# Performance work log

Measured on AMD Instinct MI355X. Metric: run time of the kernel, lower is better.

Reference implementation:

```python
import jax, jax.numpy as jnp
import numpy as np

B, N_H, N_W, DIM, HEADS = 2, 64, 64, 768, 12
HINT = 1024
HIDDEN = DIM * 2       # LTRM expand_ratio = 2
K_ECA = 5              # ECA kernel for C=768: int(|log2(768)/2 + 0.5|)=5 (odd)
TH_LO, TH_HI, MIN_EDGE = 0.02, 0.98, 64


def setup_inputs() -> dict:
    key = jax.random.key(0)
    ks = jax.random.split(key, 12)
    N = N_H * N_W
    x = jax.random.normal(ks[0], (B, N, DIM), jnp.float32)
    # alpha hint: left half = uniform noise (uncertain -> edge tokens),
    # right half = binary blocks aligned to the 16px token cells (easy tokens)
    blocks = (jax.random.uniform(ks[1], (B, 1, N_H, N_W)) > 0.5).astype(jnp.float32)
    blocks_up = jnp.repeat(jnp.repeat(blocks, HINT // N_H, axis=2), HINT // N_W, axis=3)
    noise = jax.random.uniform(ks[2], (B, 1, HINT, HINT))
    col = jnp.arange(HINT)[None, None, None, :]
    alpha_hint = jnp.where(col < HINT // 2, noise, blocks_up)
    s = 0.02
    return {
        "x": x,
        "alpha_hint": alpha_hint,
        # global attention (Hiera-style patched MaskUnitAttention, q_stride=1)
        "qkv_w": jax.random.normal(ks[3], (DIM, 3 * DIM), jnp.float32) * s,
        "qkv_b": jnp.zeros((3 * DIM,), jnp.float32),
        "proj_w": jax.random.normal(ks[4], (DIM, DIM), jnp.float32) * s,
        "proj_b": jnp.zeros((DIM,), jnp.float32),
        # LTRM
        "ln_g": jnp.ones((DIM,), jnp.float32),
        "ln_b": jnp.zeros((DIM,), jnp.float32),
        "fc1_w": jax.random.normal(ks[5], (DIM, HIDDEN), jnp.float32) * s,
        "fc1_b": jnp.zeros((HIDDEN,), jnp.float32),
        "fc2_w": jax.random.normal(ks[6], (HIDDEN, DIM), jnp.float32) * s,  # zeros in ckpt; random for non-trivial math
        "fc2_b": jnp.zeros((DIM,), jnp.float32),
        "eca_w": jax.random.normal(ks[7], (K_ECA,), jnp.float32) * 0.2,
    }


def _edge_mask(alpha_hint):
    # F.interpolate(mode='area') with exact integer factor == block mean
    Bn = alpha_hint.shape[0]
    f_h, f_w = HINT // N_H, HINT // N_W
    hint = alpha_hint.reshape(Bn, N_H, f_h, N_W, f_w).mean(axis=(2, 4)).reshape(Bn, N_H * N_W)
    edge = (hint > TH_LO) & (hint < TH_HI)
    # per-batch fallback: too few edge tokens -> route everything to attention
    edge = jnp.where(edge.sum(axis=1, keepdims=True) < MIN_EDGE, True, edge)
    return edge  # [B, N] bool


def _layernorm(h, g, b, eps=1e-5):
    mu = h.mean(-1, keepdims=True)
    var = ((h - mu) ** 2).mean(-1, keepdims=True)
    return (h - mu) * jax.lax.rsqrt(var + eps) * g + b


def reference(x, alpha_hint, qkv_w, qkv_b, proj_w, proj_b,
              ln_g, ln_b, fc1_w, fc1_b, fc2_w, fc2_b, eca_w):
    Bn, N, C = x.shape
    hd = C // HEADS
    edge = _edge_mask(alpha_hint)                      # [B, N] bool

    # ---- edge path: global SDPA restricted to edge tokens (masked form of
    # the gather->attend->scatter routing: same math, edge keys only) ----
    qkv = (x @ qkv_w + qkv_b).reshape(Bn, N, 3, HEADS, hd)
    q = qkv[:, :, 0].transpose(0, 2, 1, 3)             # [B,H,N,hd]
    k = qkv[:, :, 1].transpose(0, 2, 1, 3)
    v = qkv[:, :, 2].transpose(0, 2, 1, 3)
    scores = jnp.einsum('bhqd,bhkd->bhqk', q, k) / jnp.sqrt(jnp.asarray(hd, x.dtype))
    scores = scores + jnp.where(edge[:, None, None, :], 0.0, -1e9).astype(x.dtype)
    attn = jax.nn.softmax(scores, axis=-1)
    o = jnp.einsum('bhqk,bhkd->bhqd', attn, v)
    o = o.transpose(0, 2, 1, 3).reshape(Bn, N, C)
    attn_out = x + (o @ proj_w + proj_b)               # residual around attention

    # ---- easy path: LTRM (subset of tokens -> DWConv branch skipped,
    # exactly as in LTRM.forward when N != H*W) ----
    h = _layernorm(x, ln_g, ln_b)
    h = jax.nn.gelu(h @ fc1_w + fc1_b, approximate=False)
    h = jax.nn.gelu(h, approximate=False)
    h = h @ fc2_w + fc2_b                              # [B,N,C]
    # ECA: avg-pool over the routed (easy) token set -> masked mean
    easy = ~edge
    cnt = jnp.maximum(easy.sum(axis=1).astype(x.dtype), 1.0)      # [B]
    pooled = (h * easy[..., None]).sum(axis=1) / cnt[:, None]     # [B,C]
    g = jax.lax.conv_general_dilated(
        pooled[:, None, :], eca_w.reshape(1, 1, K_ECA), (1,), 'SAME',
        dimension_numbers=('NCH', 'OIH', 'NCH'))[:, 0, :]          # [B,C]
    h = h * jax.nn.sigmoid(g)[:, None, :]
    ltrm_out = x + h

    # ---- scatter-combine ----
    return jnp.where(edge[..., None], attn_out, ltrm_out)
```

## Files before the change

kernel.cpp:

```cpp
#include <hip/hip_runtime.h>

using u16 = unsigned short;
using short8 = __attribute__((ext_vector_type(8))) short;
using f32x4 = __attribute__((ext_vector_type(4))) float;

#define NTOK 4096
#define CDIM 768
#define QKVD 2304
#define NHEAD 12

__device__ __forceinline__ u16 f2bf(float f) {
  unsigned u = __float_as_uint(f);
  u += 0x7FFFu + ((u >> 16) & 1u);
  return (u16)(u >> 16);
}

__device__ __forceinline__ void gload_lds16(const void* g, void* l) {
  __builtin_amdgcn_global_load_lds(
      (__attribute__((address_space(1))) void*)g,
      (__attribute__((address_space(3))) void*)l, 16u, 0, 0u);
}

__device__ __forceinline__ float gelu_exact(float z) {
  return 0.5f * z * (1.0f + erff(z * 0.70710678118654752f));
}

__global__ __launch_bounds__(256) void pool_hint_kernel(
    const float* __restrict__ ah, float* __restrict__ hint)
{
  const int bid = blockIdx.x;
  const int b = bid >> 6, cr = bid & 63;
  const int t = threadIdx.x;
  const float* base = ah + ((size_t)b * 1024 + (size_t)cr * 16) * 1024;
  float s = 0.f;
#pragma unroll
  for (int pr = 0; pr < 16; ++pr) {
    float4 v = *(const float4*)(base + (size_t)pr * 1024 + t * 4);
    s += v.x + v.y + v.z + v.w;
  }
  s += __shfl_xor(s, 1);
  s += __shfl_xor(s, 2);
  if ((t & 3) == 0)
    hint[b * NTOK + cr * 64 + (t >> 2)] = s * (1.f / 256.f);
}

__global__ __launch_bounds__(1024) void finalize_edge_kernel(
    const float* __restrict__ hint, int* __restrict__ edge,
    int* __restrict__ qidx, int* __restrict__ ecnt)
{
  const int b = blockIdx.x, t = threadIdx.x;
  __shared__ int wsum[16];
  __shared__ int scnt;
  __shared__ int stot;
  int bits[4]; int s = 0;
#pragma unroll
  for (int j = 0; j < 4; ++j) {
    float h = hint[b * NTOK + t * 4 + j];
    bits[j] = (h > 0.02f && h < 0.98f) ? 1 : 0;
    s += bits[j];
    qidx[b * NTOK + t * 4 + j] = -1;
  }
  int sw = s;
#pragma unroll
  for (int d = 1; d < 64; d <<= 1) sw += __shfl_xor(sw, d);
  const int l = t & 63, w = t >> 6;
  if (l == 0) wsum[w] = sw;
  if (t == 0) scnt = 0;
  __syncthreads();
  if (t == 0) { int a = 0; for (int i = 0; i < 16; ++i) a += wsum[i]; stot = a; }
  __syncthreads();
  const int cnt = stot;
  const bool fb = cnt < 64;
#pragma unroll
  for (int j = 0; j < 4; ++j) {
    int e = fb ? 1 : bits[j];
    edge[b * NTOK + t * 4 + j] = e;
    if (e) {
      int p = atomicAdd(&scnt, 1);
      qidx[b * NTOK + p] = t * 4 + j;
    }
  }
  if (t == 0) ecnt[b] = fb ? 0 : (NTOK - cnt);
}

__global__ __launch_bounds__(256) void ln_kernel(
    const float* __restrict__ x, const float* __restrict__ gam,
    const float* __restrict__ bet, u16* __restrict__ lnb, u16* __restrict__ xb)
{
  const int row = blockIdx.x, t = threadIdx.x;
  const float* xr = x + (size_t)row * CDIM;
  float v[3];
#pragma unroll
  for (int j = 0; j < 3; ++j) v[j] = xr[t + j * 256];
  float s = v[0] + v[1] + v[2];
  float ss = v[0] * v[0] + v[1] * v[1] + v[2] * v[2];
#pragma unroll
  for (int d = 1; d < 64; d <<= 1) { s += __shfl_xor(s, d); ss += __shfl_xor(ss, d); }
  __shared__ float red[8];
  const int l = t & 63, w = t >> 6;
  if (l == 0) { red[w * 2] = s; red[w * 2 + 1] = ss; }
  __syncthreads();
  s = red[0] + red[2] + red[4] + red[6];
  ss = red[1] + red[3] + red[5] + red[7];
  const float mu = s * (1.f / 768.f);
  const float rstd = rsqrtf(ss * (1.f / 768.f) - mu * mu + 1e-5f);
#pragma unroll
  for (int j = 0; j < 3; ++j) {
    const int cc = t + j * 256;
    lnb[(size_t)row * CDIM + cc] = f2bf((v[j] - mu) * rstd * gam[cc] + bet[cc]);
    xb[(size_t)row * CDIM + cc] = f2bf(v[j]);
  }
}

__global__ __launch_bounds__(256) void transpose_kernel(
    const float* __restrict__ in, u16* __restrict__ outp, int K, int N)
{
  __shared__ float tile[32][33];
  const int bx = blockIdx.x, by = blockIdx.y;
  const int tx = threadIdx.x & 31, ty = threadIdx.x >> 5;
#pragma unroll
  for (int j = 0; j < 32; j += 8)
    tile[ty + j][tx] = in[(size_t)(by * 32 + ty + j) * N + bx * 32 + tx];
  __syncthreads();
#pragma unroll
  for (int j = 0; j < 32; j += 8)
    outp[(size_t)(bx * 32 + ty + j) * K + by * 32 + tx] = f2bf(tile[tx][ty + j]);
}

template <int EPI>
__global__ __launch_bounds__(256) void gemm_bt(
    const u16* __restrict__ A, const u16* __restrict__ Bt,
    const float* __restrict__ bias, const float* __restrict__ resid,
    void* __restrict__ outp, int M, int N, int K)
{
  __shared__ __align__(16) u16 lA[128 * 32];
  __shared__ __align__(16) u16 lB[128 * 32];
  const int t = threadIdx.x;
  const int l = t & 63, w = t >> 6;
  const int g = l >> 4, c = l & 15;
  const int wr = w >> 1, wc = w & 1;
  const int bm = blockIdx.x, bn = blockIdx.y;

  f32x4 acc[4][4];
#pragma unroll
  for (int i = 0; i < 4; ++i)
#pragma unroll
    for (int j = 0; j < 4; ++j) acc[i][j] = f32x4{0.f, 0.f, 0.f, 0.f};

  const int srow = t >> 2;
  const int sslot = (t & 3) ^ (srow & 3);
  const u16* gA0 = A + (size_t)(bm * 128 + srow) * K + sslot * 8;
  const u16* gA1 = A + (size_t)(bm * 128 + 64 + srow) * K + sslot * 8;
  const u16* gB0 = Bt + (size_t)(bn * 128 + srow) * K + sslot * 8;
  const u16* gB1 = Bt + (size_t)(bn * 128 + 64 + srow) * K + sslot * 8;
  char* ldA = (char*)lA + w * 1024;
  char* ldB = (char*)lB + w * 1024;

  for (int k0 = 0; k0 < K; k0 += 32) {
    __syncthreads();
    gload_lds16(gA0 + k0, ldA);
    gload_lds16(gA1 + k0, ldA + 4096);
    gload_lds16(gB0 + k0, ldB);
    gload_lds16(gB1 + k0, ldB + 4096);
    __syncthreads();
    short8 af[4], bfr[4];
#pragma unroll
    for (int mi = 0; mi < 4; ++mi) {
      int row = wr * 64 + mi * 16 + c;
      af[mi] = *(const short8*)((const char*)lA + row * 64 + ((g ^ (row & 3)) << 4));
    }
#pragma unroll
    for (int ni = 0; ni < 4; ++ni) {
      int row = wc * 64 + ni * 16 + c;
      bfr[ni] = *(const short8*)((const char*)lB + row * 64 + ((g ^ (row & 3)) << 4));
    }
#pragma unroll
    for (int mi = 0; mi < 4; ++mi)
#pragma unroll
      for (int ni = 0; ni < 4; ++ni)
        acc[mi][ni] = __builtin_amdgcn_mfma_f32_16x16x32_bf16(af[mi], bfr[ni], acc[mi][ni], 0, 0, 0);
  }

#pragma unroll
  for (int mi = 0; mi < 4; ++mi) {
#pragma unroll
    for (int ni = 0; ni < 4; ++ni) {
      const int col = bn * 128 + wc * 64 + ni * 16 + c;
      const float bv = bias[col];
      const int row0 = bm * 128 + wr * 64 + mi * 16 + g * 4;
#pragma unroll
      for (int r = 0; r < 4; ++r) {
        float v = acc[mi][ni][r] + bv;
        const size_t idx = (size_t)(row0 + r) * N + col;
        if constexpr (EPI == 0) {
          ((u16*)outp)[idx] = f2bf(v);
        } else if constexpr (EPI == 1) {
          ((float*)outp)[idx] = v + resid[idx];
        } else if constexpr (EPI == 2) {
          ((u16*)outp)[idx] = f2bf(gelu_exact(gelu_exact(v)));
        } else {
          ((float*)outp)[idx] = v;
        }
      }
    }
  }
}

__global__ __launch_bounds__(256) void flash_kernel(
    const u16* __restrict__ qkv, const int* __restrict__ qidx, u16* __restrict__ o)
{
  const int qt = blockIdx.x;
  const int bh = blockIdx.y;
  const int b = bh / NHEAD, h = bh % NHEAD;
  const int* qx = qidx + b * NTOK;
  if (qx[qt * 128] < 0) return;

  __shared__ __align__(16) u16 lK[64 * 64];
  __shared__ __align__(16) u16 lV[64 * 64];
  __shared__ __align__(16) u16 lP[4][32 * 64];

  const int t = threadIdx.x;
  const int l = t & 63, w = t >> 6;
  const int g = l >> 4, c = l & 15;
  const size_t tokbase = (size_t)b * NTOK;

  short8 qf[2][2];
#pragma unroll
  for (int mi = 0; mi < 2; ++mi) {
    int qi = qx[qt * 128 + w * 32 + mi * 16 + c];
    if (qi < 0) qi = 0;
    const u16* qp = qkv + (tokbase + qi) * QKVD + h * 64;
#pragma unroll
    for (int kb = 0; kb < 2; ++kb)
      qf[mi][kb] = *(const short8*)(qp + kb * 32 + g * 8);
  }

  f32x4 oacc[2][4];
  float mrun[2][4], lrun[2][4];
#pragma unroll
  for (int mi = 0; mi < 2; ++mi) {
#pragma unroll
    for (int nd = 0; nd < 4; ++nd) oacc[mi][nd] = f32x4{0.f, 0.f, 0.f, 0.f};
#pragma unroll
    for (int r = 0; r < 4; ++r) { mrun[mi][r] = -1e30f; lrun[mi][r] = 0.f; }
  }

  u16* lPw = lP[w];

  for (int kt = 0; kt < NTOK / 64; ++kt) {
    if (qx[kt * 64] < 0) break;
    __syncthreads();
#pragma unroll
    for (int j = 0; j < 2; ++j) {
      int seg = j * 256 + t;
      int row = seg >> 3;
      int sl = (seg & 7) ^ (row & 7);
      int ki = qx[kt * 64 + row]; if (ki < 0) ki = 0;
      gload_lds16(qkv + (tokbase + ki) * QKVD + CDIM + h * 64 + sl * 8,
                  (char*)lK + j * 4096 + w * 1024);
    }
    {
      int vi = qx[kt * 64 + l]; if (vi < 0) vi = 0;
      const u16* vg = qkv + (tokbase + vi) * QKVD + 2 * CDIM + h * 64 + w * 16;
      union { uint4 q[2]; u16 s[16]; } vv;
      vv.q[0] = *(const uint4*)(vg);
      vv.q[1] = *(const uint4*)(vg + 8);
#pragma unroll
      for (int jj = 0; jj < 16; ++jj) {
        int d = w * 16 + jj;
        *(u16*)((char*)lV + d * 128 + ((l * 2) ^ ((d & 7) << 4))) = vv.s[jj];
      }
    }
    __syncthreads();

    short8 kf[4][2];
#pragma unroll
    for (int ni = 0; ni < 4; ++ni) {
      int row = ni * 16 + c;
#pragma unroll
      for (int kb = 0; kb < 2; ++kb)
        kf[ni][kb] = *(const short8*)((const char*)lK + row * 128 + (((kb * 4 + g) ^ (row & 7)) << 4));
    }
    f32x4 s[2][4];
#pragma unroll
    for (int mi = 0; mi < 2; ++mi)
#pragma unroll
      for (int ni = 0; ni < 4; ++ni) {
        f32x4 sv = f32x4{0.f, 0.f, 0.f, 0.f};
        sv = __builtin_amdgcn_mfma_f32_16x16x32_bf16(qf[mi][0], kf[ni][0], sv, 0, 0, 0);
        sv = __builtin_amdgcn_mfma_f32_16x16x32_bf16(qf[mi][1], kf[ni][1], sv, 0, 0, 0);
        s[mi][ni] = sv;
      }

    float emask[4];
#pragma unroll
    for (int ni = 0; ni < 4; ++ni)
      emask[ni] = (qx[kt * 64 + ni * 16 + c] >= 0) ? 0.f : -1e9f;

#pragma unroll
    for (int mi = 0; mi < 2; ++mi) {
      float mx[4];
#pragma unroll
      for (int r = 0; r < 4; ++r) {
        float a0 = s[mi][0][r] * 0.125f + emask[0];
        float a1 = s[mi][1][r] * 0.125f + emask[1];
        float a2 = s[mi][2][r] * 0.125f + emask[2];
        float a3 = s[mi][3][r] * 0.125f + emask[3];
        s[mi][0][r] = a0; s[mi][1][r] = a1; s[mi][2][r] = a2; s[mi][3][r] = a3;
        mx[r] = fmaxf(fmaxf(a0, a1), fmaxf(a2, a3));
      }
#pragma unroll
      for (int r = 0; r < 4; ++r)
#pragma unroll
        for (int d = 1; d < 16; d <<= 1)
          mx[r] = fmaxf(mx[r], __shfl_xor(mx[r], d));

      float alpha[4], rs[4];
#pragma unroll
      for (int r = 0; r < 4; ++r) {
        float mnew = fmaxf(mrun[mi][r], mx[r]);
        alpha[r] = __expf(mrun[mi][r] - mnew);
        mrun[mi][r] = mnew;
        float accp = 0.f;
        const int prow = mi * 16 + g * 4 + r;
#pragma unroll
        for (int ni = 0; ni < 4; ++ni) {
          float p = __expf(s[mi][ni][r] - mnew);
          accp += p;
          *(u16*)((char*)lPw + prow * 128 + (((ni * 16 + c) * 2) ^ ((prow & 7) << 4))) = f2bf(p);
        }
        rs[r] = accp;
      }
#pragma unroll
      for (int r = 0; r < 4; ++r)
#pragma unroll
        for (int d = 1; d < 16; d <<= 1) rs[r] += __shfl_xor(rs[r], d);
#pragma unroll
      for (int r = 0; r < 4; ++r) {
        lrun[mi][r] = lrun[mi][r] * alpha[r] + rs[r];
#pragma unroll
        for (int nd = 0; nd < 4; ++nd) oacc[mi][nd][r] *= alpha[r];
      }
    }

#pragma unroll
    for (int kb = 0; kb < 2; ++kb) {
      short8 pa[2], vf[4];
#pragma unroll
      for (int mi = 0; mi < 2; ++mi) {
        int prow = mi * 16 + c;
        pa[mi] = *(const short8*)((const char*)lPw + prow * 128 + (((kb * 4 + g) ^ (prow & 7)) << 4));
      }
#pragma unroll
      for (int nd = 0; nd < 4; ++nd) {
        int vrow = nd * 16 + c;
        vf[nd] = *(const short8*)((const char*)lV + vrow * 128 + (((kb * 4 + g) ^ (vrow & 7)) << 4));
      }
#pragma unroll
      for (int mi = 0; mi < 2; ++mi)
#pragma unroll
        for (int nd = 0; nd < 4; ++nd)
          oacc[mi][nd] = __builtin_amdgcn_mfma_f32_16x16x32_bf16(pa[mi], vf[nd], oacc[mi][nd], 0, 0, 0);
    }
  }

#pragma unroll
  for (int mi = 0; mi < 2; ++mi) {
    float inv[4];
#pragma unroll
    for (int r = 0; r < 4; ++r) inv[r] = 1.f / lrun[mi][r];
#pragma unroll
    for (int r = 0; r < 4; ++r) {
      int oi = qx[qt * 128 + w * 32 + mi * 16 + g * 4 + r];
      if (oi >= 0) {
        u16* op = o + (tokbase + oi) * CDIM + h * 64;
#pragma unroll
        for (int nd = 0; nd < 4; ++nd)
          op[nd * 16 + c] = f2bf(oacc[mi][nd][r] * inv[r]);
      }
    }
  }
}

__global__ __launch_bounds__(256) void pool_partial_kernel(
    const float* __restrict__ h2, const int* __restrict__ edge, float* __restrict__ pooled)
{
  const int bid = blockIdx.x;
  const int b = bid / 48, rm = bid % 48;
  const int cg = rm / 16, ts = rm % 16;
  const int ch = cg * 256 + threadIdx.x;
  float s = 0.f;
  for (int tok = ts * 256; tok < ts * 256 + 256; ++tok) {
    if (!edge[b * NTOK + tok])
      s += h2[((size_t)b * NTOK + tok) * CDIM + ch];
  }
  atomicAdd(&pooled[b * CDIM + ch], s);
}

__global__ void eca_kernel(const float* __restrict__ pooled, const float* __restrict__ w5,
                           const int* __restrict__ ecnt, float* __restrict__ gate)
{
  const int b = blockIdx.x, c = threadIdx.x;
  const float inv = 1.f / fmaxf((float)ecnt[b], 1.f);
  float a = 0.f;
#pragma unroll
  for (int j = 0; j < 5; ++j) {
    int i = c - 2 + j;
    if (i >= 0 && i < CDIM) a += w5[j] * pooled[b * CDIM + i];
  }
  a *= inv;
  gate[b * CDIM + c] = 1.f / (1.f + __expf(-a));
}

__global__ __launch_bounds__(256) void combine_kernel(
    const float* __restrict__ x, const float* __restrict__ attn,
    const float* __restrict__ h2, const float* __restrict__ gate,
    const int* __restrict__ edge, float* __restrict__ out)
{
  const size_t i = ((size_t)blockIdx.x * 256 + threadIdx.x) * 4;
  const int b = (int)(i / ((size_t)NTOK * CDIM));
  const size_t r = i % ((size_t)NTOK * CDIM);
  const int tok = (int)(r / CDIM);
  const int cc = (int)(r % CDIM);
  float4 ov;
  if (edge[b * NTOK + tok]) {
    ov = *(const float4*)(attn + i);
  } else {
    float4 xv = *(const float4*)(x + i);
    float4 hv = *(const float4*)(h2 + i);
    float4 gv = *(const float4*)(gate + b * CDIM + cc);
    ov.x = xv.x + hv.x * gv.x;
    ov.y = xv.y + hv.y * gv.y;
    ov.z = xv.z + hv.z * gv.z;
    ov.w = xv.w + hv.w * gv.w;
  }
  *(float4*)(out + i) = ov;
}

extern "C" void kernel_launch(void* const* d_in, const int* in_sizes, int n_in,
                              void* d_out, int out_size, void* d_ws, size_t ws_size,
                              hipStream_t stream) {
  const float* x      = (const float*)d_in[0];
  const float* ah     = (const float*)d_in[1];
  const float* qkv_w  = (const float*)d_in[2];
  const float* qkv_b  = (const float*)d_in[3];
  const float* proj_w = (const float*)d_in[4];
  const float* proj_b = (const float*)d_in[5];
  const float* ln_g   = (const float*)d_in[6];
  const float* ln_b   = (const float*)d_in[7];
  const float* fc1_w  = (const float*)d_in[8];
  const float* fc1_b  = (const float*)d_in[9];
  const float* fc2_w  = (const float*)d_in[10];
  const float* fc2_b  = (const float*)d_in[11];
  const float* eca_w  = (const float*)d_in[12];
  float* out = (float*)d_out;

  char* ws = (char*)d_ws;
  size_t off = 0;
  auto alloc = [&](size_t bytes) {
    char* p = ws + off;
    off += (bytes + 255) & ~(size_t)255;
    return p;
  };
  float* hint   = (float*)alloc((size_t)2 * NTOK * 4);
  int*   edge   = (int*)alloc((size_t)2 * NTOK * 4);
  int*   qidx   = (int*)alloc((size_t)2 * NTOK * 4);
  int*   ecnt   = (int*)alloc(256);
  u16*   xbf    = (u16*)alloc((size_t)2 * NTOK * CDIM * 2);
  u16*   lnbf   = (u16*)alloc((size_t)2 * NTOK * CDIM * 2);
  u16*   qkvT   = (u16*)alloc((size_t)QKVD * CDIM * 2);
  u16*   projT  = (u16*)alloc((size_t)CDIM * CDIM * 2);
  u16*   fc1T   = (u16*)alloc((size_t)1536 * CDIM * 2);
  u16*   fc2T   = (u16*)alloc((size_t)CDIM * 1536 * 2);
  u16*   qkvb   = (u16*)alloc((size_t)2 * NTOK * QKVD * 2);
  u16*   obf    = (u16*)alloc((size_t)2 * NTOK * CDIM * 2);
  u16*   h1bf   = (u16*)alloc((size_t)2 * NTOK * 1536 * 2);
  float* h2     = (float*)alloc((size_t)2 * NTOK * CDIM * 4);
  float* attn   = (float*)alloc((size_t)2 * NTOK * CDIM * 4);
  float* pooled = (float*)alloc((size_t)2 * CDIM * 4);
  float* gate   = (float*)alloc((size_t)2 * CDIM * 4);

  pool_hint_kernel<<<dim3(128), 256, 0, stream>>>(ah, hint);
  finalize_edge_kernel<<<dim3(2), 1024, 0, stream>>>(hint, edge, qidx, ecnt);
  ln_kernel<<<dim3(8192), 256, 0, stream>>>(x, ln_g, ln_b, lnbf, xbf);
  transpose_kernel<<<dim3(72, 24), 256, 0, stream>>>(qkv_w, qkvT, 768, 2304);
  transpose_kernel<<<dim3(24, 24), 256, 0, stream>>>(proj_w, projT, 768, 768);
  transpose_kernel<<<dim3(48, 24), 256, 0, stream>>>(fc1_w, fc1T, 768, 1536);
  transpose_kernel<<<dim3(24, 48), 256, 0, stream>>>(fc2_w, fc2T, 1536, 768);

  gemm_bt<0><<<dim3(64, 18), 256, 0, stream>>>(xbf, qkvT, qkv_b, nullptr, qkvb, 8192, 2304, 768);
  flash_kernel<<<dim3(32, 24), 256, 0, stream>>>(qkvb, qidx, obf);
  gemm_bt<1><<<dim3(64, 6), 256, 0, stream>>>(obf, projT, proj_b, x, attn, 8192, 768, 768);
  gemm_bt<2><<<dim3(64, 12), 256, 0, stream>>>(lnbf, fc1T, fc1_b, nullptr, h1bf, 8192, 1536, 768);
  gemm_bt<3><<<dim3(64, 6), 256, 0, stream>>>(h1bf, fc2T, fc2_b, nullptr, h2, 8192, 768, 1536);

  hipMemsetAsync(pooled, 0, (size_t)2 * CDIM * 4, stream);
  pool_partial_kernel<<<dim3(96), 256, 0, stream>>>(h2, edge, pooled);
  eca_kernel<<<dim3(2), 768, 0, stream>>>(pooled, eca_w, ecnt, gate);
  combine_kernel<<<dim3(6144), 256, 0, stream>>>(x, attn, h2, gate, edge, out);
}
```

Baseline: 553.3 us.

## Compact edge/easy token lists so GEMMs skip unused rows; split-KV flash attention

Token routing now builds two compacted index lists, one for edge tokens and one for easy tokens. The QKV and fc1 GEMMs gather only the routed rows, and the proj and fc2 GEMMs scatter results back by token index. Tiles with no routed rows exit early, which roughly halves the matmul work. Flash attention now reads the compacted QKV contiguously and splits the key range into two partitions, adding a merge kernel that combines partial outputs with their max and sum statistics. The trade-off is extra partial-output buffers, an extra launch and list indirection inside the GEMM loads and epilogues.

```diff
diff --git a/kernel.cpp b/kernel.cpp
--- a/kernel.cpp
+++ b/kernel.cpp
@@ -13,6 +13,9 @@
   unsigned u = __float_as_uint(f);
   u += 0x7FFFu + ((u >> 16) & 1u);
   return (u16)(u >> 16);
+}
+__device__ __forceinline__ float bf2f(u16 v) {
+  return __uint_as_float(((unsigned)v) << 16);
 }
 
 __device__ __forceinline__ void gload_lds16(const void* g, void* l) {
@@ -46,12 +49,12 @@
 
 __global__ __launch_bounds__(1024) void finalize_edge_kernel(
     const float* __restrict__ hint, int* __restrict__ edge,
-    int* __restrict__ qidx, int* __restrict__ ecnt)
+    int* __restrict__ qidx, int* __restrict__ eidx,
+    int* __restrict__ cntE, int* __restrict__ cntZ)
 {
   const int b = blockIdx.x, t = threadIdx.x;
   __shared__ int wsum[16];
-  __shared__ int scnt;
-  __shared__ int stot;
+  __shared__ int scntE, scntZ, stot;
   int bits[4]; int s = 0;
 #pragma unroll
   for (int j = 0; j < 4; ++j) {
@@ -59,28 +62,32 @@
     bits[j] = (h > 0.02f && h < 0.98f) ? 1 : 0;
     s += bits[j];
     qidx[b * NTOK + t * 4 + j] = -1;
+    eidx[b * NTOK + t * 4 + j] = -1;
   }
   int sw = s;
 #pragma unroll
   for (int d = 1; d < 64; d <<= 1) sw += __shfl_xor(sw, d);
   const int l = t & 63, w = t >> 6;
   if (l == 0) wsum[w] = sw;
-  if (t == 0) scnt = 0;
+  if (t == 0) { scntE = 0; scntZ = 0; }
   __syncthreads();
   if (t == 0) { int a = 0; for (int i = 0; i < 16; ++i) a += wsum[i]; stot = a; }
   __syncthreads();
-  const int cnt = stot;
-  const bool fb = cnt < 64;
+  const bool fb = stot < 64;
 #pragma unroll
   for (int j = 0; j < 4; ++j) {
     int e = fb ? 1 : bits[j];
     edge[b * NTOK + t * 4 + j] = e;
     if (e) {
-      int p = atomicAdd(&scnt, 1);
+      int p = atomicAdd(&scntE, 1);
       qidx[b * NTOK + p] = t * 4 + j;
-    }
-  }
-  if (t == 0) ecnt[b] = fb ? 0 : (NTOK - cnt);
+    } else {
+      int p = atomicAdd(&scntZ, 1);
+      eidx[b * NTOK + p] = t * 4 + j;
+    }
+  }
+  __syncthreads();
+  if (t == 0) { cntE[b] = scntE; cntZ[b] = scntZ; }
 }
 
 __global__ __launch_bounds__(256) void ln_kernel(
@@ -127,19 +134,23 @@
     outp[(size_t)(bx * 32 + ty + j) * K + by * 32 + tx] = f2bf(tile[tx][ty + j]);
 }
 
-template <int EPI>
+template <int EPI, bool GATHER_A, bool SCATTER_OUT>
 __global__ __launch_bounds__(256) void gemm_bt(
     const u16* __restrict__ A, const u16* __restrict__ Bt,
     const float* __restrict__ bias, const float* __restrict__ resid,
-    void* __restrict__ outp, int M, int N, int K)
-{
+    const int* __restrict__ list, void* __restrict__ outp, int N, int K)
+{
+  const int bm = blockIdx.x, bn = blockIdx.y;
+  const int b = bm >> 5, bmi = bm & 31;
+  const int rb = bmi * 128;
+  if (list[b * NTOK + rb] < 0) return;
+
   __shared__ __align__(16) u16 lA[128 * 32];
   __shared__ __align__(16) u16 lB[128 * 32];
   const int t = threadIdx.x;
   const int l = t & 63, w = t >> 6;
   const int g = l >> 4, c = l & 15;
   const int wr = w >> 1, wc = w & 1;
-  const int bm = blockIdx.x, bn = blockIdx.y;
 
   f32x4 acc[4][4];
 #pragma unroll
@@ -149,8 +160,16 @@
 
   const int srow = t >> 2;
   const int sslot = (t & 3) ^ (srow & 3);
-  const u16* gA0 = A + (size_t)(bm * 128 + srow) * K + sslot * 8;
-  const u16* gA1 = A + (size_t)(bm * 128 + 64 + srow) * K + sslot * 8;
+  int ta0, ta1;
+  if constexpr (GATHER_A) {
+    ta0 = list[b * NTOK + rb + srow];       if (ta0 < 0) ta0 = 0;
+    ta1 = list[b * NTOK + rb + 64 + srow];  if (ta1 < 0) ta1 = 0;
+  } else {
+    ta0 = rb + srow;
+    ta1 = rb + 64 + srow;
+  }
+  const u16* gA0 = A + ((size_t)b * NTOK + ta0) * K + sslot * 8;
+  const u16* gA1 = A + ((size_t)b * NTOK + ta1) * K + sslot * 8;
   const u16* gB0 = Bt + (size_t)(bn * 128 + srow) * K + sslot * 8;
   const u16* gB1 = Bt + (size_t)(bn * 128 + 64 + srow) * K + sslot * 8;
   char* ldA = (char*)lA + w * 1024;
@@ -187,11 +206,19 @@
     for (int ni = 0; ni < 4; ++ni) {
       const int col = bn * 128 + wc * 64 + ni * 16 + c;
       const float bv = bias[col];
-      const int row0 = bm * 128 + wr * 64 + mi * 16 + g * 4;
+      const int prow0 = rb + wr * 64 + mi * 16 + g * 4;
 #pragma unroll
       for (int r = 0; r < 4; ++r) {
         float v = acc[mi][ni][r] + bv;
-        const size_t idx = (size_t)(row0 + r) * N + col;
+        int orow;
+        if constexpr (SCATTER_OUT) {
+          int tok = list[b * NTOK + prow0 + r];
+          if (tok < 0) continue;
+          orow = tok;
+        } else {
+          orow = prow0 + r;
+        }
+        const size_t idx = ((size_t)b * NTOK + orow) * N + col;
         if constexpr (EPI == 0) {
           ((u16*)outp)[idx] = f2bf(v);
         } else if constexpr (EPI == 1) {
@@ -206,14 +233,22 @@
   }
 }
 
-__global__ __launch_bounds__(256) void flash_kernel(
-    const u16* __restrict__ qkv, const int* __restrict__ qidx, u16* __restrict__ o)
+#define NSPLIT 2
+__global__ __launch_bounds__(256) void flash_part_kernel(
+    const u16* __restrict__ qkv, const int* __restrict__ cntE,
+    u16* __restrict__ partO, float2* __restrict__ partML)
 {
   const int qt = blockIdx.x;
   const int bh = blockIdx.y;
+  const int sp = blockIdx.z;
   const int b = bh / NHEAD, h = bh % NHEAD;
-  const int* qx = qidx + b * NTOK;
-  if (qx[qt * 128] < 0) return;
+  const int cnt = cntE[b];
+  if (qt * 128 >= cnt) return;
+
+  const int ntiles = (cnt + 63) >> 6;
+  const int half = (ntiles + NSPLIT - 1) / NSPLIT;
+  const int tA = sp * half;
+  const int tB = min(ntiles, tA + half);
 
   __shared__ __align__(16) u16 lK[64 * 64];
   __shared__ __align__(16) u16 lV[64 * 64];
@@ -227,9 +262,8 @@
   short8 qf[2][2];
 #pragma unroll
   for (int mi = 0; mi < 2; ++mi) {
-    int qi = qx[qt * 128 + w * 32 + mi * 16 + c];
-    if (qi < 0) qi = 0;
-    const u16* qp = qkv + (tokbase + qi) * QKVD + h * 64;
+    const int pos = qt * 128 + w * 32 + mi * 16 + c;
+    const u16* qp = qkv + (tokbase + pos) * QKVD + h * 64;
 #pragma unroll
     for (int kb = 0; kb < 2; ++kb)
       qf[mi][kb] = *(const short8*)(qp + kb * 32 + g * 8);
@@ -247,28 +281,27 @@
 
   u16* lPw = lP[w];
 
-  for (int kt = 0; kt < NTOK / 64; ++kt) {
-    if (qx[kt * 64] < 0) break;
+  for (int kt = tA; kt < tB; ++kt) {
     __syncthreads();
 #pragma unroll
     for (int j = 0; j < 2; ++j) {
       int seg = j * 256 + t;
       int row = seg >> 3;
       int sl = (seg & 7) ^ (row & 7);
-      int ki = qx[kt * 64 + row]; if (ki < 0) ki = 0;
-      gload_lds16(qkv + (tokbase + ki) * QKVD + CDIM + h * 64 + sl * 8,
+      gload_lds16(qkv + (tokbase + kt * 64 + row) * QKVD + CDIM + h * 64 + sl * 8,
                   (char*)lK + j * 4096 + w * 1024);
     }
     {
-      int vi = qx[kt * 64 + l]; if (vi < 0) vi = 0;
-      const u16* vg = qkv + (tokbase + vi) * QKVD + 2 * CDIM + h * 64 + w * 16;
-      union { uint4 q[2]; u16 s[16]; } vv;
-      vv.q[0] = *(const uint4*)(vg);
-      vv.q[1] = *(const uint4*)(vg + 8);
-#pragma unroll
-      for (int jj = 0; jj < 16; ++jj) {
-        int d = w * 16 + jj;
-        *(u16*)((char*)lV + d * 128 + ((l * 2) ^ ((d & 7) << 4))) = vv.s[jj];
+      const int kp = t & 31, db = t >> 5;
+      const u16* vg = qkv + (tokbase + kt * 64 + kp * 2) * QKVD + 2 * CDIM + h * 64 + db * 8;
+      union { uint4 q; u16 s[8]; } v0, v1;
+      v0.q = *(const uint4*)vg;
+      v1.q = *(const uint4*)(vg + QKVD);
+#pragma unroll
+      for (int j = 0; j < 8; ++j) {
+        int d = db * 8 + j;
+        unsigned pk = (unsigned)v0.s[j] | ((unsigned)v1.s[j] << 16);
+        *(unsigned*)((char*)lV + d * 128 + ((kp * 4) ^ ((d & 7) << 4))) = pk;
       }
     }
     __syncthreads();
@@ -295,7 +328,7 @@
     float emask[4];
 #pragma unroll
     for (int ni = 0; ni < 4; ++ni)
-      emask[ni] = (qx[kt * 64 + ni * 16 + c] >= 0) ? 0.f : -1e9f;
+      emask[ni] = (kt * 64 + ni * 16 + c < cnt) ? 0.f : -1e9f;
 
 #pragma unroll
     for (int mi = 0; mi < 2; ++mi) {
@@ -364,22 +397,44 @@
     }
   }
 
+  const size_t pobase = ((size_t)(sp * 2 + b) * NHEAD + h) * NTOK;
 #pragma unroll
   for (int mi = 0; mi < 2; ++mi) {
-    float inv[4];
-#pragma unroll
-    for (int r = 0; r < 4; ++r) inv[r] = 1.f / lrun[mi][r];
 #pragma unroll
     for (int r = 0; r < 4; ++r) {
-      int oi = qx[qt * 128 + w * 32 + mi * 16 + g * 4 + r];
-      if (oi >= 0) {
-        u16* op = o + (tokbase + oi) * CDIM + h * 64;
+      const int pos = qt * 128 + w * 32 + mi * 16 + g * 4 + r;
+      if (pos < cnt) {
+        u16* op = partO + (pobase + pos) * 64;
 #pragma unroll
         for (int nd = 0; nd < 4; ++nd)
-          op[nd * 16 + c] = f2bf(oacc[mi][nd][r] * inv[r]);
-      }
-    }
-  }
+          op[nd * 16 + c] = f2bf(oacc[mi][nd][r]);
+        if (c == 0)
+          partML[pobase + pos] = make_float2(mrun[mi][r], lrun[mi][r]);
+      }
+    }
+  }
+}
+
+__global__ __launch_bounds__(256) void flash_merge_kernel(
+    const u16* __restrict__ partO, const float2* __restrict__ partML,
+    const int* __restrict__ cntE, u16* __restrict__ obf)
+{
+  const int bh = blockIdx.y;
+  const int b = bh / NHEAD, h = bh % NHEAD;
+  const int t = threadIdx.x;
+  const int pos = blockIdx.x * 4 + (t >> 6);
+  const int d = t & 63;
+  if (pos >= cntE[b]) return;
+  const size_t p0 = ((size_t)(0 * 2 + b) * NHEAD + h) * NTOK + pos;
+  const size_t p1 = ((size_t)(1 * 2 + b) * NHEAD + h) * NTOK + pos;
+  const float2 ml0 = partML[p0];
+  const float2 ml1 = partML[p1];
+  const float M = fmaxf(ml0.x, ml1.x);
+  const float e0 = __expf(ml0.x - M);
+  const float e1 = __expf(ml1.x - M);
+  const float L = ml0.y * e0 + ml1.y * e1;
+  const float o = (e0 * bf2f(partO[p0 * 64 + d]) + e1 * bf2f(partO[p1 * 64 + d])) / L;
+  obf[((size_t)b * NTOK + pos) * CDIM + h * 64 + d] = f2bf(o);
 }
 
 __global__ __launch_bounds__(256) void pool_partial_kernel(
@@ -465,7 +520,9 @@
   float* hint   = (float*)alloc((size_t)2 * NTOK * 4);
   int*   edge   = (int*)alloc((size_t)2 * NTOK * 4);
   int*   qidx   = (int*)alloc((size_t)2 * NTOK * 4);
-  int*   ecnt   = (int*)alloc(256);
+  int*   eidx   = (int*)alloc((size_t)2 * NTOK * 4);
+  int*   cntE   = (int*)alloc(256);
+  int*   cntZ   = (int*)alloc(256);
   u16*   xbf    = (u16*)alloc((size_t)2 * NTOK * CDIM * 2);
   u16*   lnbf   = (u16*)alloc((size_t)2 * NTOK * CDIM * 2);
   u16*   qkvT   = (u16*)alloc((size_t)QKVD * CDIM * 2);
@@ -477,25 +534,32 @@
   u16*   h1bf   = (u16*)alloc((size_t)2 * NTOK * 1536 * 2);
   float* h2     = (float*)alloc((size_t)2 * NTOK * CDIM * 4);
   float* attn   = (float*)alloc((size_t)2 * NTOK * CDIM * 4);
+  u16*   partO  = (u16*)alloc((size_t)NSPLIT * 2 * NHEAD * NTOK * 64 * 2);
+  float* partML = (float*)alloc((size_t)NSPLIT * 2 * NHEAD * NTOK * 8);
   float* pooled = (float*)alloc((size_t)2 * CDIM * 4);
   float* gate   = (float*)alloc((size_t)2 * CDIM * 4);
 
   pool_hint_kernel<<<dim3(128), 256, 0, stream>>>(ah, hint);
-  finalize_edge_kernel<<<dim3(2), 1024, 0, stream>>>(hint, edge, qidx, ecnt);
+  finalize_edge_kernel<<<dim3(2), 1024, 0, stream>>>(hint, edge, qidx, eidx, cntE, cntZ);
   ln_kernel<<<dim3(8192), 256, 0, stream>>>(x, ln_g, ln_b, lnbf, xbf);
   transpose_kernel<<<dim3(72, 24), 256, 0, stream>>>(qkv_w, qkvT, 768, 2304);
   transpose_kernel<<<dim3(24, 24), 256, 0, stream>>>(proj_w, projT, 768, 768);
   transpose_kernel<<<dim3(48, 24), 256, 0, stream>>>(fc1_w, fc1T, 768, 1536);
   transpose_kernel<<<dim3(24, 48), 256, 0, stream>>>(fc2_w, fc2T, 1536, 768);
 
-  gemm_bt<0><<<dim3(64, 18), 256, 0, stream>>>(xbf, qkvT, qkv_b, nullptr, qkvb, 8192, 2304, 768);
-  flash_kernel<<<dim3(32, 24), 256, 0, stream>>>(qkvb, qidx, obf);
-  gemm_bt<1><<<dim3(64, 6), 256, 0, stream>>>(obf, projT, proj_b, x, attn, 8192, 768, 768);
-  gemm_bt<2><<<dim3(64, 12), 256, 0, stream>>>(lnbf, fc1T, fc1_b, nullptr, h1bf, 8192, 1536, 768);
-  gemm_bt<3><<<dim3(64, 6), 256, 0, stream>>>(h1bf, fc2T, fc2_b, nullptr, h2, 8192, 768, 1536);
+  gemm_bt<0, true, false><<<dim3(64, 18), 256, 0, stream>>>(
+      xbf, qkvT, qkv_b, nullptr, qidx, qkvb, 2304, 768);
+  flash_part_kernel<<<dim3(32, 24, NSPLIT), 256, 0, stream>>>(qkvb, cntE, partO, (float2*)partML);
+  flash_merge_kernel<<<dim3(1024, 24), 256, 0, stream>>>(partO, (const float2*)partML, cntE, obf);
+  gemm_bt<1, false, true><<<dim3(64, 6), 256, 0, stream>>>(
+      obf, projT, proj_b, x, qidx, attn, 768, 768);
+  gemm_bt<2, true, false><<<dim3(64, 12), 256, 0, stream>>>(
+      lnbf, fc1T, fc1_b, nullptr, eidx, h1bf, 1536, 768);
+  gemm_bt<3, false, true><<<dim3(64, 6), 256, 0, stream>>>(
+      h1bf, fc2T, fc2_b, nullptr, eidx, h2, 768, 1536);
 
   hipMemsetAsync(pooled, 0, (size_t)2 * CDIM * 4, stream);
   pool_partial_kernel<<<dim3(96), 256, 0, stream>>>(h2, edge, pooled);
-  eca_kernel<<<dim3(2), 768, 0, stream>>>(pooled, eca_w, ecnt, gate);
+  eca_kernel<<<dim3(2), 768, 0, stream>>>(pooled, eca_w, cntZ, gate);
   combine_kernel<<<dim3(6144), 256, 0, stream>>>(x, attn, h2, gate, edge, out);
 }
```

New measurement: 542.3 us. 2.0% less time.
